# Kernel tuning notes

Hardware: AMD Instinct MI355X
Metric: run time of the kernel (lower is better)

## Reference

```python
import jax, jax.numpy as jnp
import numpy as np

VOCAB = 8192  # upper bound on integer values appearing in features


def setup_inputs() -> dict:
    key = jax.random.key(0)
    # [B, L] integer codes; each row is treated as a SET of values (duplicates ignored)
    features = jax.random.randint(key, (4096, 256), 0, VOCAB, dtype=jnp.int32)
    return {"features": features}


def reference(features) -> jnp.ndarray:
    # np.intersect1d / np.union1d compute set intersection/union of unique values.
    # Equivalent vectorized form: binary presence matrix P[i, v] = 1 iff value v in row i.
    B, L = features.shape
    rows = jnp.arange(B)[:, None]                                  # [B, 1]
    presence = jnp.zeros((B, VOCAB), jnp.float32).at[rows, features].set(1.0)  # [B, V]
    inter = presence @ presence.T                                  # [B, B] |A_i & A_j|
    sizes = presence.sum(axis=1)                                   # [B]    |A_i|
    union = sizes[:, None] + sizes[None, :] - inter                # [B, B] |A_i | A_j|
    # original returns -intersection/union (note the negation), 0 when union == 0
    sim = jnp.where(union != 0, -inter / jnp.where(union != 0, union, 1.0), 0.0)
    return sim
```

## Files before the change

kernel.cpp:

```cpp
#include <hip/hip_runtime.h>
#include <stdint.h>

#define B_ROWS 4096
#define L_FEAT 256
#define VOCAB  8192
#define ROWB   (VOCAB / 2)
#define BM 128
#define BN 128
#define BKE 128
#define BKB 64
#define NSTEP (VOCAB / BKE)

typedef __attribute__((ext_vector_type(4)))  int   intx4;
typedef __attribute__((ext_vector_type(8)))  int   intx8;
typedef __attribute__((ext_vector_type(4)))  float floatx4;
typedef __attribute__((ext_vector_type(16))) float floatx16;

__device__ __forceinline__ void async_copy16(const void* gsrc, void* ldst) {
  __builtin_amdgcn_global_load_lds(
      (const __attribute__((address_space(1))) void*)gsrc,
      (__attribute__((address_space(3))) void*)ldst, 16, 0, 0);
}

__global__ __launch_bounds__(256) void presence_kernel(
    const int* __restrict__ f,
    uint32_t* __restrict__ P,
    float* __restrict__ sizes) {
  __shared__ uint32_t rw[4][VOCAB / 8];
  const int rbase = blockIdx.x * 4;
  const int tid = threadIdx.x;

  uint4* rp4 = (uint4*)&rw[0][0];
  const uint4 z = make_uint4(0u, 0u, 0u, 0u);
  #pragma unroll
  for (int j = 0; j < 4; ++j) rp4[tid + j * 256] = z;
  __syncthreads();

  #pragma unroll
  for (int r = 0; r < 4; ++r) {
    const int v = f[(rbase + r) * L_FEAT + tid];
    atomicOr(&rw[r][v >> 3], 0x2u << ((v & 7) * 4));
  }
  __syncthreads();

  const int w = tid >> 6, lane = tid & 63;
  uint4* op4 = (uint4*)(P + (size_t)(rbase + w) * (ROWB / 4));
  const uint4* sp4 = (const uint4*)&rw[w][0];
  int cnt = 0;
  #pragma unroll
  for (int q = 0; q < 4; ++q) {
    const uint4 x = sp4[lane + q * 64];
    op4[lane + q * 64] = x;
    cnt += __popc(x.x & 0x22222222u) + __popc(x.y & 0x22222222u) +
           __popc(x.z & 0x22222222u) + __popc(x.w & 0x22222222u);
  }
  #pragma unroll
  for (int off = 32; off > 0; off >>= 1) cnt += __shfl_down(cnt, off);
  if (lane == 0) sizes[rbase + w] = (float)cnt;
}

__global__ __launch_bounds__(256, 3) void gemm_kernel(
    const unsigned char* __restrict__ P,
    const float* __restrict__ sizes,
    float* __restrict__ out) {
  int bid = blockIdx.x;
  bid = (bid & 7) * 66 + (bid >> 3);
  int b = bid, by = 0, rem = 32;
  while (b >= rem) { b -= rem; ++by; --rem; }
  const int bx = by + b;
  const int iBase = by * BM;
  const int jBase = bx * BN;

  __shared__ __align__(16) unsigned char As[3][8192];
  __shared__ __align__(16) unsigned char Bs[3][8192];

  const int tid  = threadIdx.x;
  const int wave = tid >> 6, lane = tid & 63;
  const int wm = wave >> 1, wn = wave & 1;
  const int r31 = lane & 31, khalf = lane >> 5;

  floatx16 acc[2][2];
  #pragma unroll
  for (int ai = 0; ai < 2; ++ai)
    #pragma unroll
    for (int ci = 0; ci < 2; ++ci)
      #pragma unroll
      for (int e = 0; e < 16; ++e) acc[ai][ci][e] = 0.f;

  const int c0 = wave, c1 = wave + 4;
  const unsigned char* srcA0 =
      P + (size_t)(iBase + (c0 >> 1) * 32 + r31) * ROWB + (c0 & 1) * 32 + khalf * 16;
  const unsigned char* srcA1 =
      P + (size_t)(iBase + (c1 >> 1) * 32 + r31) * ROWB + (c1 & 1) * 32 + khalf * 16;
  const unsigned char* srcB0 =
      P + (size_t)(jBase + (c0 >> 1) * 32 + r31) * ROWB + (c0 & 1) * 32 + khalf * 16;
  const unsigned char* srcB1 =
      P + (size_t)(jBase + (c1 >> 1) * 32 + r31) * ROWB + (c1 & 1) * 32 + khalf * 16;

  #define STAGE(buf, k0b)                                                     \
    {                                                                         \
      async_copy16(srcA0 + (k0b), &As[buf][c0 * 1024]);                       \
      async_copy16(srcA1 + (k0b), &As[buf][c1 * 1024]);                       \
      async_copy16(srcB0 + (k0b), &Bs[buf][c0 * 1024]);                       \
      async_copy16(srcB1 + (k0b), &Bs[buf][c1 * 1024]);                       \
    }

  STAGE(0, 0);
  STAGE(1, BKB);

  int cur = 0, pre = 2;
  for (int i = 0; i < NSTEP; ++i) {
    asm volatile("s_waitcnt vmcnt(4)" ::: "memory");
    __builtin_amdgcn_s_barrier();

    STAGE(pre, ((i + 2) * BKB) & (ROWB - 1));

    intx4 a4[2][2], b4[2][2];
    #pragma unroll
    for (int t = 0; t < 2; ++t)
      #pragma unroll
      for (int kk = 0; kk < 2; ++kk) {
        a4[t][kk] = *(const intx4*)
            &As[cur][((wm * 2 + t) * 2 + kk) * 1024 + lane * 16];
        b4[t][kk] = *(const intx4*)
            &Bs[cur][((wn * 2 + t) * 2 + kk) * 1024 + lane * 16];
      }

    __builtin_amdgcn_s_setprio(1);
    #pragma unroll
    for (int kk = 0; kk < 2; ++kk)
      #pragma unroll
      for (int tm = 0; tm < 2; ++tm)
        #pragma unroll
        for (int tn = 0; tn < 2; ++tn) {
          intx8 a8, b8;
          #pragma unroll
          for (int e = 0; e < 4; ++e) {
            a8[e] = a4[tm][kk][e];  a8[e + 4] = 0;
            b8[e] = b4[tn][kk][e];  b8[e + 4] = 0;
          }
          acc[tm][tn] = __builtin_amdgcn_mfma_scale_f32_32x32x64_f8f6f4(
              a8, b8, acc[tm][tn],
              4, 4,
              0, 127,
              0, 127);
        }
    __builtin_amdgcn_s_setprio(0);

    cur = (cur == 2) ? 0 : cur + 1;
    pre = (pre == 2) ? 0 : pre + 1;
  }

  #pragma unroll
  for (int tm = 0; tm < 2; ++tm) {
    const int rowb = iBase + wm * 64 + tm * 32 + 4 * khalf;
    #pragma unroll
    for (int tn = 0; tn < 2; ++tn) {
      const int colb = jBase + wn * 64 + tn * 32 + r31;
      const float sj = sizes[colb];
      #pragma unroll
      for (int q = 0; q < 4; ++q) {
        const int rq = rowb + 8 * q;
        floatx4 tv;
        #pragma unroll
        for (int j = 0; j < 4; ++j) {
          const float inter = acc[tm][tn][4 * q + j];
          const float u = sizes[rq + j] + sj - inter;
          tv[j] = (u != 0.f) ? (-inter / u) : 0.f;
        }
        __builtin_nontemporal_store(tv[0], &out[(size_t)(rq + 0) * B_ROWS + colb]);
        __builtin_nontemporal_store(tv[1], &out[(size_t)(rq + 1) * B_ROWS + colb]);
        __builtin_nontemporal_store(tv[2], &out[(size_t)(rq + 2) * B_ROWS + colb]);
        __builtin_nontemporal_store(tv[3], &out[(size_t)(rq + 3) * B_ROWS + colb]);
        __builtin_nontemporal_store(tv, (floatx4*)&out[(size_t)colb * B_ROWS + rq]);
      }
    }
  }
}

extern "C" void kernel_launch(void* const* d_in, const int* in_sizes, int n_in,
                              void* d_out, int out_size, void* d_ws, size_t ws_size,
                              hipStream_t stream) {
  const int* features = (const int*)d_in[0];
  float* out = (float*)d_out;
  uint32_t* P = (uint32_t*)d_ws;
  float* sizes = (float*)((char*)d_ws + (size_t)B_ROWS * ROWB);

  presence_kernel<<<B_ROWS / 4, 256, 0, stream>>>(features, P, sizes);
  gemm_kernel<<<528, 256, 0, stream>>>((const unsigned char*)P, sizes, out);
}
```

Baseline: 206.4 us.

## Load MFMA operands directly from global into registers, drop LDS staging

Removes the LDS triple-buffered async staging and barriers from the GEMM. Each wave now loads its own A and B fragments straight from global memory into a 4-deep register ring, with a prefetch distance of 3. The FP4 operand is widened by duplicating the 16 bytes instead of zero-padding. This removes the barrier and LDS round-trip overhead, but each wave now reads its tiles independently, so global/L2 traffic is duplicated across waves and loads are 16-byte strided per row. The widen duplication changes the upper operand half, which is fine only if the MFMA ignores it under the fp4 format.

```diff
diff --git a/kernel.cpp b/kernel.cpp
--- a/kernel.cpp
+++ b/kernel.cpp
@@ -5,21 +5,15 @@
 #define L_FEAT 256
 #define VOCAB  8192
 #define ROWB   (VOCAB / 2)
-#define BM 128
-#define BN 128
-#define BKE 128
-#define BKB 64
-#define NSTEP (VOCAB / BKE)
+#define NSTEP  128
 
 typedef __attribute__((ext_vector_type(4)))  int   intx4;
 typedef __attribute__((ext_vector_type(8)))  int   intx8;
 typedef __attribute__((ext_vector_type(4)))  float floatx4;
 typedef __attribute__((ext_vector_type(16))) float floatx16;
 
-__device__ __forceinline__ void async_copy16(const void* gsrc, void* ldst) {
-  __builtin_amdgcn_global_load_lds(
-      (const __attribute__((address_space(1))) void*)gsrc,
-      (__attribute__((address_space(3))) void*)ldst, 16, 0, 0);
+__device__ __forceinline__ intx8 widen(intx4 v) {
+  return __builtin_shufflevector(v, v, 0, 1, 2, 3, 0, 1, 2, 3);
 }
 
 __global__ __launch_bounds__(256) void presence_kernel(
@@ -68,16 +62,19 @@
   int b = bid, by = 0, rem = 32;
   while (b >= rem) { b -= rem; ++by; --rem; }
   const int bx = by + b;
-  const int iBase = by * BM;
-  const int jBase = bx * BN;
-
-  __shared__ __align__(16) unsigned char As[3][8192];
-  __shared__ __align__(16) unsigned char Bs[3][8192];
 
   const int tid  = threadIdx.x;
   const int wave = tid >> 6, lane = tid & 63;
   const int wm = wave >> 1, wn = wave & 1;
   const int r31 = lane & 31, khalf = lane >> 5;
+
+  const int iB = by * 128 + wm * 64;
+  const int jB = bx * 128 + wn * 64;
+
+  const unsigned char* pA0 = P + (size_t)(iB + r31) * ROWB + khalf * 16;
+  const unsigned char* pA1 = pA0 + (size_t)32 * ROWB;
+  const unsigned char* pB0 = P + (size_t)(jB + r31) * ROWB + khalf * 16;
+  const unsigned char* pB1 = pB0 + (size_t)32 * ROWB;
 
   floatx16 acc[2][2];
   #pragma unroll
@@ -87,76 +84,47 @@
       #pragma unroll
       for (int e = 0; e < 16; ++e) acc[ai][ci][e] = 0.f;
 
-  const int c0 = wave, c1 = wave + 4;
-  const unsigned char* srcA0 =
-      P + (size_t)(iBase + (c0 >> 1) * 32 + r31) * ROWB + (c0 & 1) * 32 + khalf * 16;
-  const unsigned char* srcA1 =
-      P + (size_t)(iBase + (c1 >> 1) * 32 + r31) * ROWB + (c1 & 1) * 32 + khalf * 16;
-  const unsigned char* srcB0 =
-      P + (size_t)(jBase + (c0 >> 1) * 32 + r31) * ROWB + (c0 & 1) * 32 + khalf * 16;
-  const unsigned char* srcB1 =
-      P + (size_t)(jBase + (c1 >> 1) * 32 + r31) * ROWB + (c1 & 1) * 32 + khalf * 16;
+  intx4 a0[4], a1[4], b0[4], b1[4];
 
-  #define STAGE(buf, k0b)                                                     \
-    {                                                                         \
-      async_copy16(srcA0 + (k0b), &As[buf][c0 * 1024]);                       \
-      async_copy16(srcA1 + (k0b), &As[buf][c1 * 1024]);                       \
-      async_copy16(srcB0 + (k0b), &Bs[buf][c0 * 1024]);                       \
-      async_copy16(srcB1 + (k0b), &Bs[buf][c1 * 1024]);                       \
+  #pragma unroll
+  for (int k = 0; k < 3; ++k) {
+    a0[k] = *(const intx4*)(pA0 + k * 32);
+    a1[k] = *(const intx4*)(pA1 + k * 32);
+    b0[k] = *(const intx4*)(pB0 + k * 32);
+    b1[k] = *(const intx4*)(pB1 + k * 32);
+  }
+
+  #pragma unroll
+  for (int k = 0; k < NSTEP; ++k) {
+    if (k + 3 < NSTEP) {
+      const int s = (k + 3) & 3;
+      const int off = (k + 3) * 32;
+      a0[s] = *(const intx4*)(pA0 + off);
+      a1[s] = *(const intx4*)(pA1 + off);
+      b0[s] = *(const intx4*)(pB0 + off);
+      b1[s] = *(const intx4*)(pB1 + off);
     }
-
-  STAGE(0, 0);
-  STAGE(1, BKB);
-
-  int cur = 0, pre = 2;
-  for (int i = 0; i < NSTEP; ++i) {
-    asm volatile("s_waitcnt vmcnt(4)" ::: "memory");
-    __builtin_amdgcn_s_barrier();
-
-    STAGE(pre, ((i + 2) * BKB) & (ROWB - 1));
-
-    intx4 a4[2][2], b4[2][2];
-    #pragma unroll
-    for (int t = 0; t < 2; ++t)
-      #pragma unroll
-      for (int kk = 0; kk < 2; ++kk) {
-        a4[t][kk] = *(const intx4*)
-            &As[cur][((wm * 2 + t) * 2 + kk) * 1024 + lane * 16];
-        b4[t][kk] = *(const intx4*)
-            &Bs[cur][((wn * 2 + t) * 2 + kk) * 1024 + lane * 16];
-      }
-
+    const int s = k & 3;
+    const intx8 A0 = widen(a0[s]), A1 = widen(a1[s]);
+    const intx8 B0 = widen(b0[s]), B1 = widen(b1[s]);
     __builtin_amdgcn_s_setprio(1);
-    #pragma unroll
-    for (int kk = 0; kk < 2; ++kk)
-      #pragma unroll
-      for (int tm = 0; tm < 2; ++tm)
-        #pragma unroll
-        for (int tn = 0; tn < 2; ++tn) {
-          intx8 a8, b8;
-          #pragma unroll
-          for (int e = 0; e < 4; ++e) {
-            a8[e] = a4[tm][kk][e];  a8[e + 4] = 0;
-            b8[e] = b4[tn][kk][e];  b8[e + 4] = 0;
-          }
-          acc[tm][tn] = __builtin_amdgcn_mfma_scale_f32_32x32x64_f8f6f4(
-              a8, b8, acc[tm][tn],
-              4, 4,
-              0, 127,
-              0, 127);
-        }
+    acc[0][0] = __builtin_amdgcn_mfma_scale_f32_32x32x64_f8f6f4(
+        A0, B0, acc[0][0], 4, 4, 0, 127, 0, 127);
+    acc[0][1] = __builtin_amdgcn_mfma_scale_f32_32x32x64_f8f6f4(
+        A0, B1, acc[0][1], 4, 4, 0, 127, 0, 127);
+    acc[1][0] = __builtin_amdgcn_mfma_scale_f32_32x32x64_f8f6f4(
+        A1, B0, acc[1][0], 4, 4, 0, 127, 0, 127);
+    acc[1][1] = __builtin_amdgcn_mfma_scale_f32_32x32x64_f8f6f4(
+        A1, B1, acc[1][1], 4, 4, 0, 127, 0, 127);
     __builtin_amdgcn_s_setprio(0);
-
-    cur = (cur == 2) ? 0 : cur + 1;
-    pre = (pre == 2) ? 0 : pre + 1;
   }
 
   #pragma unroll
   for (int tm = 0; tm < 2; ++tm) {
-    const int rowb = iBase + wm * 64 + tm * 32 + 4 * khalf;
+    const int rowb = iB + tm * 32 + 4 * khalf;
     #pragma unroll
     for (int tn = 0; tn < 2; ++tn) {
-      const int colb = jBase + wn * 64 + tn * 32 + r31;
+      const int colb = jB + tn * 32 + r31;
       const float sj = sizes[colb];
       #pragma unroll
       for (int q = 0; q < 4; ++q) {
```

After: 417.9 us. +102.5%, slower.

## Switch GEMM LDS pipeline from triple to double buffering with per-step barrier

Applied to the files above, without the earlier changes.

Shrinks the async global-to-LDS staging from three buffers to two and prefetches only one step ahead. Each iteration issues the next stage right after reading the current buffer and ends with a full __syncthreads. It also drops the min-blocks occupancy hint from the launch bounds and builds the MFMA operands by duplicating the 4-dword fp4 vector instead of zero-padding it. Smaller LDS use may allow more resident blocks, but the shallower prefetch and full barrier each step risk exposing global load latency.

```diff
diff --git a/kernel.cpp b/kernel.cpp
--- a/kernel.cpp
+++ b/kernel.cpp
@@ -15,6 +15,10 @@
 typedef __attribute__((ext_vector_type(8)))  int   intx8;
 typedef __attribute__((ext_vector_type(4)))  float floatx4;
 typedef __attribute__((ext_vector_type(16))) float floatx16;
+
+__device__ __forceinline__ intx8 widen(intx4 v) {
+  return __builtin_shufflevector(v, v, 0, 1, 2, 3, 0, 1, 2, 3);
+}
 
 __device__ __forceinline__ void async_copy16(const void* gsrc, void* ldst) {
   __builtin_amdgcn_global_load_lds(
@@ -59,7 +63,7 @@
   if (lane == 0) sizes[rbase + w] = (float)cnt;
 }
 
-__global__ __launch_bounds__(256, 3) void gemm_kernel(
+__global__ __launch_bounds__(256) void gemm_kernel(
     const unsigned char* __restrict__ P,
     const float* __restrict__ sizes,
     float* __restrict__ out) {
@@ -71,8 +75,8 @@
   const int iBase = by * BM;
   const int jBase = bx * BN;
 
-  __shared__ __align__(16) unsigned char As[3][8192];
-  __shared__ __align__(16) unsigned char Bs[3][8192];
+  __shared__ __align__(16) unsigned char As[2][8192];
+  __shared__ __align__(16) unsigned char Bs[2][8192];
 
   const int tid  = threadIdx.x;
   const int wave = tid >> 6, lane = tid & 63;
@@ -106,15 +110,10 @@
     }
 
   STAGE(0, 0);
-  STAGE(1, BKB);
+  __syncthreads();
 
-  int cur = 0, pre = 2;
+  int cur = 0;
   for (int i = 0; i < NSTEP; ++i) {
-    asm volatile("s_waitcnt vmcnt(4)" ::: "memory");
-    __builtin_amdgcn_s_barrier();
-
-    STAGE(pre, ((i + 2) * BKB) & (ROWB - 1));
-
     intx4 a4[2][2], b4[2][2];
     #pragma unroll
     for (int t = 0; t < 2; ++t)
@@ -126,29 +125,26 @@
             &Bs[cur][((wn * 2 + t) * 2 + kk) * 1024 + lane * 16];
       }
 
+    STAGE(cur ^ 1, ((i + 1) * BKB) & (ROWB - 1));
+
     __builtin_amdgcn_s_setprio(1);
     #pragma unroll
-    for (int kk = 0; kk < 2; ++kk)
-      #pragma unroll
-      for (int tm = 0; tm < 2; ++tm)
-        #pragma unroll
-        for (int tn = 0; tn < 2; ++tn) {
-          intx8 a8, b8;
-          #pragma unroll
-          for (int e = 0; e < 4; ++e) {
-            a8[e] = a4[tm][kk][e];  a8[e + 4] = 0;
-            b8[e] = b4[tn][kk][e];  b8[e + 4] = 0;
-          }
-          acc[tm][tn] = __builtin_amdgcn_mfma_scale_f32_32x32x64_f8f6f4(
-              a8, b8, acc[tm][tn],
-              4, 4,
-              0, 127,
-              0, 127);
-        }
+    for (int kk = 0; kk < 2; ++kk) {
+      const intx8 A0 = widen(a4[0][kk]), A1 = widen(a4[1][kk]);
+      const intx8 B0 = widen(b4[0][kk]), B1 = widen(b4[1][kk]);
+      acc[0][0] = __builtin_amdgcn_mfma_scale_f32_32x32x64_f8f6f4(
+          A0, B0, acc[0][0], 4, 4, 0, 127, 0, 127);
+      acc[0][1] = __builtin_amdgcn_mfma_scale_f32_32x32x64_f8f6f4(
+          A0, B1, acc[0][1], 4, 4, 0, 127, 0, 127);
+      acc[1][0] = __builtin_amdgcn_mfma_scale_f32_32x32x64_f8f6f4(
+          A1, B0, acc[1][0], 4, 4, 0, 127, 0, 127);
+      acc[1][1] = __builtin_amdgcn_mfma_scale_f32_32x32x64_f8f6f4(
+          A1, B1, acc[1][1], 4, 4, 0, 127, 0, 127);
+    }
     __builtin_amdgcn_s_setprio(0);
 
-    cur = (cur == 2) ? 0 : cur + 1;
-    pre = (pre == 2) ? 0 : pre + 1;
+    __syncthreads();
+    cur ^= 1;
   }
 
   #pragma unroll
```

After: 224.7 us. +8.9%, slower.
